# Kernel optimization log

Hardware: AMD Instinct MI355X
Metric: run time of the kernel (lower is better)

The kernel has to match this reference:

```python
import jax, jax.numpy as jnp
import numpy as np
from functools import partial

DIM, HID, DK, NH, SEQ, B = 1024, 512, 512, 4, 16, 2048
DH = DK // NH  # per-head dim = 128
EPS = 1e-5


def _ln(x, g, b):
    m = x.mean(-1, keepdims=True)
    v = ((x - m) ** 2).mean(-1, keepdims=True)
    return (x - m) * jax.lax.rsqrt(v + EPS) * g + b


def setup_inputs() -> dict:
    key = jax.random.key(0)
    ks = jax.random.split(key, 32)
    it = iter(range(32))
    n = lambda shape, s: jax.random.normal(ks[next(it)], shape, jnp.float32) * s
    inp = {
        'visual': n((B, SEQ, DIM), 1.0),
        'text':   n((B, SEQ, DIM), 1.0),
        'user':   n((B, SEQ, DIM), 1.0),
        'cat':    n((B, SEQ, DIM), 1.0),
        'label':  n((B, SEQ, 1), 1.0),
        'h0':     n((B, HID), 1.0),
        'c0':     n((B, HID), 1.0),
        # fusion MLP: Linear(4*dim -> dim)
        'fus_W': n((DIM, 4 * DIM), 1.0 / np.sqrt(4 * DIM)),
        'fus_b': n((DIM,), 0.01),
        # LayerNormLSTM cell params (gate order i,f,g,o)
        'W_ih': n((4 * HID, DIM), 1.0 / np.sqrt(DIM)),
        'W_hh': n((4 * HID, HID), 1.0 / np.sqrt(HID)),
        'g_ih': 1.0 + n((4 * HID,), 0.1), 'b_ih': n((4 * HID,), 0.01),
        'g_hh': 1.0 + n((4 * HID,), 0.1), 'b_hh': n((4 * HID,), 0.01),
        'g_c':  1.0 + n((HID,), 0.1),     'b_c':  n((HID,), 0.01),
        # attention projections
        'wq_W': n((DK, HID), 1.0 / np.sqrt(HID)), 'wq_b': n((DK,), 0.01),
        'wk_W': n((DK, HID), 1.0 / np.sqrt(HID)), 'wk_b': n((DK,), 0.01),
        'wv_W': n((NH, DK, HID), 1.0 / np.sqrt(HID)), 'wv_b': n((NH, DK), 0.01),
        'wout_W': n((DK, DK * NH), 1.0 / np.sqrt(DK * NH)), 'wout_b': n((DK,), 0.01),
        'out_W': n((1, DK), 1.0 / np.sqrt(DK)), 'out_b': n((1,), 0.01),
    }
    return inp


def reference(visual, text, user, cat, label, h0, c0, fus_W, fus_b,
              W_ih, W_hh, g_ih, b_ih, g_hh, b_hh, g_c, b_c,
              wq_W, wq_b, wk_W, wk_b, wv_W, wv_b, wout_W, wout_b, out_W, out_b):
    # fusion MLP (dropout is identity at inference)
    mods = jnp.concatenate([visual, text, user, cat], axis=-1)  # [B,S,4*DIM]
    v_t = jax.nn.relu(mods @ fus_W.T + fus_b)                    # [B,S,DIM]

    # LayerNorm-LSTM recurrence over time via scan
    def step(carry, x_t):
        h, c = carry
        gates = _ln(x_t @ W_ih.T, g_ih, b_ih) + _ln(h @ W_hh.T, g_hh, b_hh)
        i, f, g, o = jnp.split(gates, 4, axis=-1)
        c = jax.nn.sigmoid(f) * c + jax.nn.sigmoid(i) * jnp.tanh(g)
        h = jax.nn.sigmoid(o) * jnp.tanh(_ln(c, g_c, b_c))
        return (h, c), h

    (hn, _), hs = jax.lax.scan(step, (h0, c0), jnp.swapaxes(v_t, 0, 1))
    lstm_out = jnp.swapaxes(hs, 0, 1)  # [B,S,HID]

    # multi-head dot self-attention against final hidden state
    q = (hn @ wq_W.T + wq_b).reshape(-1, NH, DH)                    # [B,H,dh]
    k = (lstm_out @ wk_W.T + wk_b).reshape(-1, SEQ, NH, DH)         # [B,S,H,dh]
    scores = jnp.einsum('bshd,bhd->bhs', k, q) / np.sqrt(DH)        # [B,H,S]
    attn = jax.nn.softmax(scores, axis=-1)
    # per-head full-width values: V[b,h,s,k]
    V = jnp.einsum('hkd,bsd->bhsk', wv_W, lstm_out) + wv_b[None, :, None, :]
    ctx = jnp.einsum('bhsk,bhs->bhk', V, attn).reshape(-1, NH * DK)  # [B,H*DK]
    out_h = ctx @ wout_W.T + wout_b                                  # [B,DK]
    output = out_h @ out_W.T + out_b                                 # [B,1]

    label_one = label[:, -1, 0]
    loss = jnp.mean((output.reshape(-1) - label_one) ** 2)
    return loss, output
```

## Files before the change

### kernel.cpp

```cpp
#include <hip/hip_runtime.h>
#include <cstdint>

#define B_SZ 2048
#define SEQ  16
#define DIM  1024
#define HID  512
#define DK   512
#define NH   4
#define DH   128
#define GATE 2048
#define EPSV 1e-5f

typedef __bf16 bf8_t __attribute__((ext_vector_type(8)));
typedef float  f4_t  __attribute__((ext_vector_type(4)));
typedef unsigned short u16x8 __attribute__((ext_vector_type(8)));
typedef unsigned short u16x4 __attribute__((ext_vector_type(4)));

__device__ __forceinline__ unsigned short f2bf(float f){
  __bf16 h = (__bf16)f;
  return __builtin_bit_cast(unsigned short, h);
}
__device__ __forceinline__ float bf2f(unsigned short u){
  return __builtin_bit_cast(float, ((unsigned int)u) << 16);
}
__device__ __forceinline__ float sigm(float x){ return 1.f/(1.f+__expf(-x)); }
__device__ __forceinline__ float tanh_f(float x){ return 1.f - 2.f/(__expf(2.f*x)+1.f); }

__device__ __forceinline__ void gload16(const void* g, void* l){
  __builtin_amdgcn_global_load_lds(
      (const __attribute__((address_space(1))) void*)g,
      (__attribute__((address_space(3))) void*)l, 16, 0, 0);
}

template<bool OUT_BF16, bool BIAS, bool RELU>
__global__ __launch_bounds__(512, 1) void gemm8p(
    const unsigned short* __restrict__ A,
    const unsigned short* __restrict__ Bw,
    const float* __restrict__ bias,
    void* __restrict__ Cp,
    int N, int K, int nwg)
{
  __shared__ __align__(16) unsigned short As[2][256*64];
  __shared__ __align__(16) unsigned short Bs[2][256*64];
  const int tid = threadIdx.x, lane = tid & 63, w = tid >> 6;
  const int bid = blockIdx.x;
  const int swz = (bid & 7)*(nwg >> 3) + (bid >> 3);
  const int nx  = N >> 8;
  const int lnx = 31 - __clz(nx);
  const int bm0 = (swz >> lnx) << 8;
  const int bn0 = (swz & (nx-1)) << 8;

  const int l8  = lane >> 3;
  const int gsw = (lane & 7) ^ l8;
  const int fr  = lane & 15, kg = lane >> 4;
  const int wm  = (w >> 2)*128, wn = (w & 3)*64;
  const int KT  = K >> 6;

  auto stA = [&](int buf, int kt, int h){
    #pragma unroll
    for (int c=0;c<2;++c){
      const int rb = h*128 + c*64 + w*8;
      gload16(A + (size_t)(bm0 + rb + l8)*K + (size_t)kt*64 + gsw*8, &As[buf][rb*64]);
    }
  };
  auto stB = [&](int buf, int kt, int h){
    #pragma unroll
    for (int c=0;c<2;++c){
      const int rb = h*128 + c*64 + w*8;
      gload16(Bw + (size_t)(bn0 + rb + l8)*K + (size_t)kt*64 + gsw*8, &Bs[buf][rb*64]);
    }
  };
  auto rdA = [&](int buf, int m, int kk)->bf8_t{
    return *(const bf8_t*)&As[buf][(wm + m*16 + fr)*64 + (((kk*4+kg) ^ (fr&7))*8)];
  };
  auto rdB = [&](int buf, int n, int kk)->bf8_t{
    return *(const bf8_t*)&Bs[buf][(wn + n*16 + fr)*64 + (((kk*4+kg) ^ (fr&7))*8)];
  };

  f4_t acc[8][4];
  #pragma unroll
  for (int m=0;m<8;++m)
    #pragma unroll
    for (int n=0;n<4;++n) acc[m][n] = (f4_t)0.f;

  bf8_t bfr[4][2];

  auto mfma2 = [&](int m0, const bf8_t a00, const bf8_t a01,
                   const bf8_t a10, const bf8_t a11){
    __builtin_amdgcn_s_setprio(1);
    #pragma unroll
    for (int n=0;n<4;++n){
      acc[m0][n]   = __builtin_amdgcn_mfma_f32_16x16x32_bf16(a00, bfr[n][0], acc[m0][n],   0,0,0);
      acc[m0][n]   = __builtin_amdgcn_mfma_f32_16x16x32_bf16(a01, bfr[n][1], acc[m0][n],   0,0,0);
      acc[m0+1][n] = __builtin_amdgcn_mfma_f32_16x16x32_bf16(a10, bfr[n][0], acc[m0+1][n], 0,0,0);
      acc[m0+1][n] = __builtin_amdgcn_mfma_f32_16x16x32_bf16(a11, bfr[n][1], acc[m0+1][n], 0,0,0);
    }
    __builtin_amdgcn_s_setprio(0);
  };

  auto phase12 = [&](int buf, auto&& stg){
    #pragma unroll
    for (int n=0;n<4;++n){ bfr[n][0]=rdB(buf,n,0); bfr[n][1]=rdB(buf,n,1); }
    const bf8_t a00=rdA(buf,0,0), a01=rdA(buf,0,1), a10=rdA(buf,1,0), a11=rdA(buf,1,1);
    stg();
    asm volatile("s_barrier" ::: "memory");
    mfma2(0, a00,a01,a10,a11);
    asm volatile("s_barrier" ::: "memory");
  };
  auto phase4 = [&](int buf, int m0, auto&& stg, bool vm){
    const bf8_t a00=rdA(buf,m0,0), a01=rdA(buf,m0,1), a10=rdA(buf,m0+1,0), a11=rdA(buf,m0+1,1);
    stg();
    if (vm){
      __builtin_amdgcn_sched_barrier(0);
      asm volatile("s_waitcnt vmcnt(4)" ::: "memory");
    }
    asm volatile("s_barrier" ::: "memory");
    mfma2(m0, a00,a01,a10,a11);
    asm volatile("s_barrier" ::: "memory");
  };

  stA(0,0,0); stA(0,0,1); stB(0,0,0); stB(0,0,1);
  stB(1,1,0); stB(1,1,1);
  __builtin_amdgcn_sched_barrier(0);
  asm volatile("s_waitcnt vmcnt(4)" ::: "memory");
  asm volatile("s_barrier" ::: "memory");

  const int NIT = KT >> 1;
  for (int it=0; it<NIT; ++it){
    const int t0 = 2*it, t1 = t0+1;
    const int tN  = (t0+2 < KT) ? t0+2 : KT-1;
    const int tB3 = (t1+2 < KT) ? t1+2 : KT-1;

    phase12(0,      [&]{ stA(1,t1,0);  });
    phase4 (0, 2,   [&]{ stA(1,t1,1);  }, false);
    phase4 (0, 4,   [&]{ stB(0,tN,0);  }, false);
    phase4 (0, 6,   [&]{ stB(0,tN,1);  }, true);
    phase12(1,      [&]{ stA(0,tN,0);  });
    phase4 (1, 2,   [&]{ stA(0,tN,1);  }, false);
    phase4 (1, 4,   [&]{ stB(1,tB3,0); }, false);
    phase4 (1, 6,   [&]{ stB(1,tB3,1); }, true);
  }

  #pragma unroll
  for (int n=0;n<4;++n){
    const int col = bn0 + wn + n*16 + fr;
    float bv = 0.f;
    if constexpr (BIAS) bv = bias[col];
    #pragma unroll
    for (int m=0;m<8;++m){
      #pragma unroll
      for (int j=0;j<4;++j){
        const int row = bm0 + wm + m*16 + kg*4 + j;
        float v = acc[m][n][j] + bv;
        if constexpr (RELU) v = fmaxf(v, 0.f);
        if constexpr (OUT_BF16) ((unsigned short*)Cp)[(size_t)row*N + col] = f2bf(v);
        else                    ((float*)Cp)[(size_t)row*N + col] = v;
      }
    }
  }
}

template<bool OUT_BF16, bool BIAS>
__global__ __launch_bounds__(256) void gemm64(
    const unsigned short* __restrict__ A,
    const unsigned short* __restrict__ Bw,
    const float* __restrict__ bias,
    void* __restrict__ Cp,
    int N, int K, int nwg)
{
  __shared__ __align__(16) unsigned short As[64*64];
  __shared__ __align__(16) unsigned short Bs[64*64];
  const int tid = threadIdx.x, lane = tid & 63, wave = tid >> 6;
  const int bid = blockIdx.x;
  const int swz = (bid & 7)*(nwg >> 3) + (bid >> 3);
  const int nx  = N >> 6;
  const int lnx = 31 - __clz(nx);
  const int bm0 = (swz >> lnx) << 6;
  const int bn0 = (swz & (nx-1)) << 6;

  const int r8  = lane >> 3;
  const int gsw = ((lane & 7) ^ r8) * 8;
  const unsigned short* Ab = A  + (size_t)(bm0 + wave*16 + r8)*K + gsw;
  const unsigned short* Bb = Bw + (size_t)(bn0 + wave*16 + r8)*K + gsw;
  unsigned short* la = As + wave*1024;
  unsigned short* lb = Bs + wave*1024;

  f4_t acc[2][2];
  #pragma unroll
  for (int m=0;m<2;++m)
    #pragma unroll
    for (int n=0;n<2;++n) acc[m][n] = (f4_t)0.f;

  const int KT = K >> 6;
  const int fr = lane & 15, kg = lane >> 4;
  const int wm = (wave & 1)*32, wn = (wave >> 1)*32;

  for (int kt = 0; kt < KT; ++kt){
    if (kt) __syncthreads();
    const size_t ko = (size_t)kt*64;
    #pragma unroll
    for (int q = 0; q < 2; ++q){
      gload16(Ab + ko + (size_t)q*8*K, la + q*512);
      gload16(Bb + ko + (size_t)q*8*K, lb + q*512);
    }
    __syncthreads();
    #pragma unroll
    for (int kk = 0; kk < 2; ++kk){
      bf8_t af[2], bf_[2];
      #pragma unroll
      for (int m=0;m<2;++m){
        const int r = wm+m*16+fr;
        af[m]  = *(const bf8_t*)&As[r*64 + (((kk*4+kg) ^ (r&7))*8)];
      }
      #pragma unroll
      for (int n=0;n<2;++n){
        const int r = wn+n*16+fr;
        bf_[n] = *(const bf8_t*)&Bs[r*64 + (((kk*4+kg) ^ (r&7))*8)];
      }
      #pragma unroll
      for (int m=0;m<2;++m)
        #pragma unroll
        for (int n=0;n<2;++n)
          acc[m][n] = __builtin_amdgcn_mfma_f32_16x16x32_bf16(af[m], bf_[n], acc[m][n], 0,0,0);
    }
  }

  #pragma unroll
  for (int n=0;n<2;++n){
    const int col = bn0 + wn + n*16 + fr;
    float bv = 0.f;
    if constexpr (BIAS) bv = bias[col];
    #pragma unroll
    for (int m=0;m<2;++m){
      #pragma unroll
      for (int j=0;j<4;++j){
        const int row = bm0 + wm + m*16 + kg*4 + j;
        float v = acc[m][n][j] + bv;
        if constexpr (OUT_BF16) ((unsigned short*)Cp)[(size_t)row*N + col] = f2bf(v);
        else                    ((float*)Cp)[(size_t)row*N + col] = v;
      }
    }
  }
}

__global__ __launch_bounds__(256) void lstm_step(
  const unsigned short* __restrict__ X, const unsigned short* __restrict__ Gh,
  const float* __restrict__ c_src, float* __restrict__ c_dst,
  const float* __restrict__ g_ih, const float* __restrict__ b_ih,
  const float* __restrict__ g_hh, const float* __restrict__ b_hh,
  const float* __restrict__ g_c,  const float* __restrict__ b_c,
  unsigned short* __restrict__ h_out, unsigned short* __restrict__ lstm_out,
  int t)
{
  const int b = blockIdx.x, tid = threadIdx.x;
  __shared__ float xs[GATE];
  __shared__ float gs[GATE];
  __shared__ float red[32];
  const unsigned short* xrow = X  + ((size_t)b*SEQ + t)*GATE;
  const unsigned short* grow = Gh + (size_t)b*GATE;
  u16x8 xv = *(const u16x8*)&xrow[tid*8];
  u16x8 gv = *(const u16x8*)&grow[tid*8];
  float sx=0,sx2=0,sg=0,sg2=0;
  #pragma unroll
  for (int j=0;j<8;++j){
    float x = bf2f(xv[j]), g = bf2f(gv[j]);
    xs[tid*8+j]=x; gs[tid*8+j]=g;
    sx += x; sx2 += x*x; sg += g; sg2 += g*g;
  }
  #pragma unroll
  for (int m=32;m;m>>=1){
    sx += __shfl_xor(sx,m); sx2 += __shfl_xor(sx2,m);
    sg += __shfl_xor(sg,m); sg2 += __shfl_xor(sg2,m);
  }
  const int w = tid>>6;
  if ((tid&63)==0){ red[w]=sx; red[4+w]=sx2; red[8+w]=sg; red[12+w]=sg2; }
  __syncthreads();
  sx  = red[0]+red[1]+red[2]+red[3];
  sx2 = red[4]+red[5]+red[6]+red[7];
  sg  = red[8]+red[9]+red[10]+red[11];
  sg2 = red[12]+red[13]+red[14]+red[15];
  const float mX = sx*(1.f/GATE), mH = sg*(1.f/GATE);
  const float rX = rsqrtf(sx2*(1.f/GATE)-mX*mX+EPSV);
  const float rH = rsqrtf(sg2*(1.f/GATE)-mH*mH+EPSV);

  float cN[2], xo[2]; float sc=0, sc2=0;
  #pragma unroll
  for (int rep=0;rep<2;++rep){
    const int n = tid + rep*256;
    const int ni=n, nf=n+HID, ng=n+2*HID, no=n+3*HID;
    float gi = (xs[ni]-mX)*rX*g_ih[ni]+b_ih[ni] + (gs[ni]-mH)*rH*g_hh[ni]+b_hh[ni];
    float gf = (xs[nf]-mX)*rX*g_ih[nf]+b_ih[nf] + (gs[nf]-mH)*rH*g_hh[nf]+b_hh[nf];
    float gg = (xs[ng]-mX)*rX*g_ih[ng]+b_ih[ng] + (gs[ng]-mH)*rH*g_hh[ng]+b_hh[ng];
    float go = (xs[no]-mX)*rX*g_ih[no]+b_ih[no] + (gs[no]-mH)*rH*g_hh[no]+b_hh[no];
    float co = c_src[(size_t)b*HID + n];
    float cn = sigm(gf)*co + sigm(gi)*tanh_f(gg);
    cN[rep]=cn; xo[rep]=go;
    sc += cn; sc2 += cn*cn;
  }
  #pragma unroll
  for (int m=32;m;m>>=1){ sc += __shfl_xor(sc,m); sc2 += __shfl_xor(sc2,m); }
  if ((tid&63)==0){ red[16+w]=sc; red[20+w]=sc2; }
  __syncthreads();
  sc  = red[16]+red[17]+red[18]+red[19];
  sc2 = red[20]+red[21]+red[22]+red[23];
  const float mC = sc*(1.f/HID);
  const float rC = rsqrtf(sc2*(1.f/HID)-mC*mC+EPSV);
  #pragma unroll
  for (int rep=0;rep<2;++rep){
    const int n = tid + rep*256;
    float hN = sigm(xo[rep])*tanh_f((cN[rep]-mC)*rC*g_c[n]+b_c[n]);
    c_dst[(size_t)b*HID+n] = cN[rep];
    unsigned short hbv = f2bf(hN);
    h_out[(size_t)b*HID+n] = hbv;
    lstm_out[((size_t)b*SEQ+t)*HID+n] = hbv;
  }
}

__global__ __launch_bounds__(256) void attn_out_k(
  const float* __restrict__ q, const unsigned short* __restrict__ Km,
  const unsigned short* __restrict__ lo_all,
  const float* __restrict__ u, const float* __restrict__ Cc,
  float* __restrict__ out)
{
  const int b = blockIdx.x, tid = threadIdx.x;
  __shared__ float qs[DK];
  __shared__ float sc[NH][SEQ];
  __shared__ float at[NH][SEQ];
  __shared__ float red[4];
  for (int i=tid; i<DK; i+=256) qs[i] = q[(size_t)b*DK + i];
  __syncthreads();
  {
    const int p = tid>>2, sub = tid&3, h = p>>4, s = p&15;
    const unsigned short* krow = Km + ((size_t)b*SEQ + s)*DK + h*DH + sub*32;
    const float* qh = &qs[h*DH + sub*32];
    float part = 0.f;
    #pragma unroll
    for (int c8=0;c8<4;++c8){
      u16x8 kv = *(const u16x8*)(krow + c8*8);
      #pragma unroll
      for (int j=0;j<8;++j) part += qh[c8*8+j]*bf2f(kv[j]);
    }
    part += __shfl_xor(part,1); part += __shfl_xor(part,2);
    if (sub==0) sc[h][s] = part * 0.08838834764831845f;
  }
  __syncthreads();
  if (tid < 64){
    const int h = tid>>4;
    float v = sc[h][tid&15], mx = v;
    #pragma unroll
    for (int m=1;m<16;m<<=1) mx = fmaxf(mx, __shfl_xor(mx,m));
    float e = __expf(v-mx), se = e;
    #pragma unroll
    for (int m=1;m<16;m<<=1) se += __shfl_xor(se,m);
    at[h][tid&15] = e/se;
  }
  __syncthreads();
  float accum = 0.f;
  #pragma unroll
  for (int it=0; it<4; ++it){
    const int idx = it*256 + tid;
    const int h = idx>>8, d0 = (idx&255)*2;
    const unsigned short* lo = lo_all + (size_t)b*SEQ*HID + d0;
    float p0=0.f, p1=0.f;
    #pragma unroll
    for (int s=0;s<16;++s){
      unsigned int pr = *(const unsigned int*)(lo + s*HID);
      float a = at[h][s];
      p0 += a*bf2f((unsigned short)(pr&0xffffu));
      p1 += a*bf2f((unsigned short)(pr>>16));
    }
    accum += u[h*HID+d0]*p0 + u[h*HID+d0+1]*p1;
  }
  #pragma unroll
  for (int m=32;m;m>>=1) accum += __shfl_xor(accum,m);
  if ((tid&63)==0) red[tid>>6] = accum;
  __syncthreads();
  if (tid==0) out[1+b] = red[0]+red[1]+red[2]+red[3] + Cc[0];
}

__global__ __launch_bounds__(256) void loss_k(const float* __restrict__ label, float* __restrict__ out){
  const int tid = threadIdx.x;
  __shared__ float red[4];
  float s = 0.f;
  for (int b=tid; b<B_SZ; b+=256){
    float d = out[1+b] - label[(size_t)b*SEQ + (SEQ-1)];
    s += d*d;
  }
  #pragma unroll
  for (int m=32;m;m>>=1) s += __shfl_xor(s,m);
  if ((tid&63)==0) red[tid>>6]=s;
  __syncthreads();
  if (tid==0) out[0] = (red[0]+red[1]+red[2]+red[3]) * (1.f/B_SZ);
}

__global__ __launch_bounds__(256) void cvt_bf16_k(const float* __restrict__ in, unsigned short* __restrict__ o, int n){
  int i = (blockIdx.x*256 + threadIdx.x)*4;
  if (i < n){
    f4_t v = *(const f4_t*)&in[i];
    u16x4 w;
    #pragma unroll
    for (int j=0;j<4;++j) w[j] = f2bf(v[j]);
    *(u16x4*)&o[i] = w;
  }
}

__global__ __launch_bounds__(256) void cvt4_k(
  const float* __restrict__ v0, const float* __restrict__ v1,
  const float* __restrict__ v2, const float* __restrict__ v3,
  unsigned short* __restrict__ dst)
{
  const int idx = blockIdx.x*256 + threadIdx.x;
  const int src = blockIdx.y;
  const float* s = src==0?v0 : src==1?v1 : src==2?v2 : v3;
  const size_t e0 = (size_t)idx*8;
  const int row = (int)(e0 >> 10);
  const int col = (int)(e0 & 1023);
  f4_t a = *(const f4_t*)&s[e0];
  f4_t b = *(const f4_t*)&s[e0+4];
  u16x8 w;
  #pragma unroll
  for (int j=0;j<4;++j){ w[j]=f2bf(a[j]); w[4+j]=f2bf(b[j]); }
  *(u16x8*)&dst[(size_t)row*4096 + src*1024 + col] = w;
}

__global__ __launch_bounds__(256) void fold_we_k(
  const float* __restrict__ wout_W, const float* __restrict__ out_W, float* __restrict__ we)
{
  const int j = blockIdx.x*256 + threadIdx.x;
  float s=0.f;
  for (int m=0;m<512;++m) s += out_W[m]*wout_W[(size_t)m*2048+j];
  we[j]=s;
}
__global__ __launch_bounds__(256) void fold_u_k(
  const float* __restrict__ we, const float* __restrict__ wv_W, float* __restrict__ u)
{
  const int o = blockIdx.x*256 + threadIdx.x;
  const int h = o>>9, d = o&511;
  const float* wv = wv_W + (size_t)h*262144 + d;
  const float* wp = we + h*512;
  float s=0.f;
  for (int k=0;k<512;++k) s += wp[k]*wv[(size_t)k*512];
  u[o]=s;
}
__global__ __launch_bounds__(256) void fold_c_k(
  const float* __restrict__ we, const float* __restrict__ wv_b,
  const float* __restrict__ out_W, const float* __restrict__ wout_b,
  const float* __restrict__ out_b, float* __restrict__ Cc)
{
  const int tid = threadIdx.x;
  __shared__ float red[4];
  float s=0.f;
  for (int j=tid;j<2048;j+=256) s += we[j]*wv_b[j];
  for (int m=tid;m<512;m+=256)  s += out_W[m]*wout_b[m];
  #pragma unroll
  for (int m=32;m;m>>=1) s += __shfl_xor(s,m);
  if ((tid&63)==0) red[tid>>6]=s;
  __syncthreads();
  if (tid==0) Cc[0] = red[0]+red[1]+red[2]+red[3] + out_b[0];
}

extern "C" void kernel_launch(void* const* d_in, const int* in_sizes, int n_in,
                              void* d_out, int out_size, void* d_ws, size_t ws_size,
                              hipStream_t stream)
{
  const float* visual = (const float*)d_in[0];
  const float* text   = (const float*)d_in[1];
  const float* user_  = (const float*)d_in[2];
  const float* cat_   = (const float*)d_in[3];
  const float* label  = (const float*)d_in[4];
  const float* h0     = (const float*)d_in[5];
  const float* c0     = (const float*)d_in[6];
  const float* fus_W  = (const float*)d_in[7];
  const float* fus_b  = (const float*)d_in[8];
  const float* W_ih   = (const float*)d_in[9];
  const float* W_hh   = (const float*)d_in[10];
  const float* g_ih   = (const float*)d_in[11];
  const float* b_ih   = (const float*)d_in[12];
  const float* g_hh   = (const float*)d_in[13];
  const float* b_hh   = (const float*)d_in[14];
  const float* g_c    = (const float*)d_in[15];
  const float* b_c    = (const float*)d_in[16];
  const float* wq_W   = (const float*)d_in[17];
  const float* wq_b   = (const float*)d_in[18];
  const float* wk_W   = (const float*)d_in[19];
  const float* wk_b   = (const float*)d_in[20];
  const float* wv_W   = (const float*)d_in[21];
  const float* wv_b   = (const float*)d_in[22];
  const float* wout_W = (const float*)d_in[23];
  const float* wout_b = (const float*)d_in[24];
  const float* out_W  = (const float*)d_in[25];
  const float* out_b  = (const float*)d_in[26];
  (void)in_sizes; (void)n_in; (void)out_size; (void)ws_size;

  char* base = (char*)d_ws; size_t off = 0;
  auto alloc = [&](size_t n)->void*{ void* p = base+off; off += n; off = (off+255)&~(size_t)255; return p; };
  unsigned short* modsB = (unsigned short*)alloc((size_t)32768*4096*2);
  unsigned short* X     = modsB;
  unsigned short* vt    = (unsigned short*)alloc((size_t)32768*1024*2);
  unsigned short* lo    = (unsigned short*)alloc((size_t)32768*512*2);
  unsigned short* Km    = (unsigned short*)alloc((size_t)32768*512*2);
  unsigned short* Gh    = (unsigned short*)alloc((size_t)2048*2048*2);
  float*          cws   = (float*)         alloc((size_t)2048*512*4);
  unsigned short* hb    = (unsigned short*)alloc((size_t)2048*512*2);
  float*          qb    = (float*)         alloc((size_t)2048*512*4);
  unsigned short* fusWb = (unsigned short*)alloc((size_t)1024*4096*2);
  unsigned short* Wihb  = (unsigned short*)alloc((size_t)2048*1024*2);
  unsigned short* Whhb  = (unsigned short*)alloc((size_t)2048*512*2);
  unsigned short* wqb   = (unsigned short*)alloc((size_t)512*512*2);
  unsigned short* wkb   = (unsigned short*)alloc((size_t)512*512*2);
  float*          we_ws = (float*)         alloc(2048*4);
  float*          u_ws  = (float*)         alloc(2048*4);
  float*          C_ws  = (float*)         alloc(256);

  cvt4_k<<<dim3(16384,4), dim3(256), 0, stream>>>(visual, text, user_, cat_, modsB);
  cvt_bf16_k<<<dim3(4096), dim3(256), 0, stream>>>(fus_W, fusWb, 1024*4096);
  cvt_bf16_k<<<dim3(2048), dim3(256), 0, stream>>>(W_ih,  Wihb,  2048*1024);
  cvt_bf16_k<<<dim3(1024), dim3(256), 0, stream>>>(W_hh,  Whhb,  2048*512);
  cvt_bf16_k<<<dim3(256),  dim3(256), 0, stream>>>(wq_W,  wqb,   512*512);
  cvt_bf16_k<<<dim3(256),  dim3(256), 0, stream>>>(wk_W,  wkb,   512*512);
  cvt_bf16_k<<<dim3(1024), dim3(256), 0, stream>>>(h0,    hb,    2048*512);
  fold_we_k<<<dim3(8), dim3(256), 0, stream>>>(wout_W, out_W, we_ws);
  fold_u_k <<<dim3(8), dim3(256), 0, stream>>>(we_ws, wv_W, u_ws);
  fold_c_k <<<dim3(1), dim3(256), 0, stream>>>(we_ws, wv_b, out_W, wout_b, out_b, C_ws);

  gemm8p<true,true,true><<<dim3(512), dim3(512), 0, stream>>>(
      modsB, fusWb, fus_b, vt, 1024, 4096, 512);
  gemm8p<true,false,false><<<dim3(1024), dim3(512), 0, stream>>>(
      vt, Wihb, nullptr, X, 2048, 1024, 1024);

  for (int t=0; t<SEQ; ++t){
    gemm64<true,false><<<dim3(1024), dim3(256), 0, stream>>>(
        hb, Whhb, nullptr, Gh, 2048, 512, 1024);
    lstm_step<<<dim3(2048), dim3(256), 0, stream>>>(
        X, Gh, (t==0 ? c0 : cws), cws, g_ih, b_ih, g_hh, b_hh, g_c, b_c, hb, lo, t);
  }

  gemm64<false,true><<<dim3(256), dim3(256), 0, stream>>>(
      hb, wqb, wq_b, qb, 512, 512, 256);
  gemm8p<true,true,false><<<dim3(256), dim3(512), 0, stream>>>(
      lo, wkb, wk_b, Km, 512, 512, 256);

  attn_out_k<<<dim3(2048), dim3(256), 0, stream>>>(qb, Km, lo, u_ws, C_ws, (float*)d_out);
  loss_k<<<dim3(1), dim3(256), 0, stream>>>(label, (float*)d_out);
}
```

Measured before the change: 1.004 ms.

## Fuse fp32-to-bf16 modality concat conversion into fusion GEMM A-tile loads

Drops the separate kernel that converted the four fp32 modality inputs into a concatenated bf16 buffer. The fusion GEMM now reads fp32 A tiles straight from the four source tensors through registers, converts them to bf16 and writes them into swizzled LDS inside the pipelined main loop. This removes one large write and re-read of a 32768x4096 bf16 intermediate. In exchange the GEMM reads A as fp32, which doubles A global traffic per tile, and adds register pressure plus conversion work to the pipeline.

Result: faster. 978.3 us (-2.6%).

```diff
diff --git a/kernel.cpp b/kernel.cpp
--- a/kernel.cpp
+++ b/kernel.cpp
@@ -155,6 +155,148 @@
         if constexpr (RELU) v = fmaxf(v, 0.f);
         if constexpr (OUT_BF16) ((unsigned short*)Cp)[(size_t)row*N + col] = f2bf(v);
         else                    ((float*)Cp)[(size_t)row*N + col] = v;
+      }
+    }
+  }
+}
+
+__global__ __launch_bounds__(512, 1) void gemm8pf(
+    const float* __restrict__ A0, const float* __restrict__ A1,
+    const float* __restrict__ A2, const float* __restrict__ A3,
+    const unsigned short* __restrict__ Bw,
+    const float* __restrict__ bias,
+    unsigned short* __restrict__ Cp,
+    int N, int K, int nwg)
+{
+  __shared__ __align__(16) unsigned short As[2][256*64];
+  __shared__ __align__(16) unsigned short Bs[2][256*64];
+  const int tid = threadIdx.x, lane = tid & 63, w = tid >> 6;
+  const int bid = blockIdx.x;
+  const int swz = (bid & 7)*(nwg >> 3) + (bid >> 3);
+  const int nx  = N >> 8;
+  const int lnx = 31 - __clz(nx);
+  const int bm0 = (swz >> lnx) << 8;
+  const int bn0 = (swz & (nx-1)) << 8;
+
+  const int l8  = lane >> 3;
+  const int gsw = (lane & 7) ^ l8;
+  const int fr  = lane & 15, kg = lane >> 4;
+  const int wm  = (w >> 2)*128, wn = (w & 3)*64;
+  const int KT  = K >> 6;
+
+  auto stB = [&](int buf, int kt, int h){
+    #pragma unroll
+    for (int c=0;c<2;++c){
+      const int rb = h*128 + c*64 + w*8;
+      gload16(Bw + (size_t)(bn0 + rb + l8)*K + (size_t)kt*64 + gsw*8, &Bs[buf][rb*64]);
+    }
+  };
+
+  f4_t rg[4];
+  auto ldA = [&](int kt, int h){
+    const int kb = kt*64, si = kb >> 10, kc = kb & 1023;
+    const float* Asel = si==0?A0 : si==1?A1 : si==2?A2 : A3;
+    const float* p = Asel + (size_t)(bm0 + h*128 + (tid>>2))*1024 + kc + (tid&3)*16;
+    rg[0] = *(const f4_t*)p;     rg[1] = *(const f4_t*)(p+4);
+    rg[2] = *(const f4_t*)(p+8); rg[3] = *(const f4_t*)(p+12);
+  };
+  auto wrA = [&](int buf, int h){
+    const int row = h*128 + (tid>>2);
+    const int s = row & 7, g0 = (tid&3)*2;
+    u16x8 w0, w1;
+    #pragma unroll
+    for (int j=0;j<4;++j){
+      w0[j]=f2bf(rg[0][j]); w0[4+j]=f2bf(rg[1][j]);
+      w1[j]=f2bf(rg[2][j]); w1[4+j]=f2bf(rg[3][j]);
+    }
+    *(u16x8*)&As[buf][row*64 + ((g0^s)*8)]     = w0;
+    *(u16x8*)&As[buf][row*64 + (((g0+1)^s)*8)] = w1;
+  };
+
+  auto rdA = [&](int buf, int m, int kk)->bf8_t{
+    return *(const bf8_t*)&As[buf][(wm + m*16 + fr)*64 + (((kk*4+kg) ^ (fr&7))*8)];
+  };
+  auto rdB = [&](int buf, int n, int kk)->bf8_t{
+    return *(const bf8_t*)&Bs[buf][(wn + n*16 + fr)*64 + (((kk*4+kg) ^ (fr&7))*8)];
+  };
+
+  f4_t acc[8][4];
+  #pragma unroll
+  for (int m=0;m<8;++m)
+    #pragma unroll
+    for (int n=0;n<4;++n) acc[m][n] = (f4_t)0.f;
+
+  bf8_t bfr[4][2];
+
+  auto mfma2 = [&](int m0, const bf8_t a00, const bf8_t a01,
+                   const bf8_t a10, const bf8_t a11){
+    __builtin_amdgcn_s_setprio(1);
+    #pragma unroll
+    for (int n=0;n<4;++n){
+      acc[m0][n]   = __builtin_amdgcn_mfma_f32_16x16x32_bf16(a00, bfr[n][0], acc[m0][n],   0,0,0);
+      acc[m0][n]   = __builtin_amdgcn_mfma_f32_16x16x32_bf16(a01, bfr[n][1], acc[m0][n],   0,0,0);
+      acc[m0+1][n] = __builtin_amdgcn_mfma_f32_16x16x32_bf16(a10, bfr[n][0], acc[m0+1][n], 0,0,0);
+      acc[m0+1][n] = __builtin_amdgcn_mfma_f32_16x16x32_bf16(a11, bfr[n][1], acc[m0+1][n], 0,0,0);
+    }
+    __builtin_amdgcn_s_setprio(0);
+  };
+
+  auto phase12 = [&](int buf, auto&& stg){
+    #pragma unroll
+    for (int n=0;n<4;++n){ bfr[n][0]=rdB(buf,n,0); bfr[n][1]=rdB(buf,n,1); }
+    const bf8_t a00=rdA(buf,0,0), a01=rdA(buf,0,1), a10=rdA(buf,1,0), a11=rdA(buf,1,1);
+    stg();
+    asm volatile("s_barrier" ::: "memory");
+    mfma2(0, a00,a01,a10,a11);
+    asm volatile("s_barrier" ::: "memory");
+  };
+  auto phase4 = [&](int buf, int m0, auto&& stg, bool vm){
+    const bf8_t a00=rdA(buf,m0,0), a01=rdA(buf,m0,1), a10=rdA(buf,m0+1,0), a11=rdA(buf,m0+1,1);
+    stg();
+    if (vm){
+      __builtin_amdgcn_sched_barrier(0);
+      asm volatile("s_waitcnt vmcnt(4)" ::: "memory");
+    }
+    asm volatile("s_barrier" ::: "memory");
+    mfma2(m0, a00,a01,a10,a11);
+    asm volatile("s_barrier" ::: "memory");
+  };
+
+  stB(0,0,0); stB(0,0,1); stB(1,1,0); stB(1,1,1);
+  ldA(0,0); wrA(0,0); ldA(0,1); wrA(0,1);
+  asm volatile("s_waitcnt lgkmcnt(0)" ::: "memory");
+  asm volatile("s_waitcnt vmcnt(0)" ::: "memory");
+  asm volatile("s_barrier" ::: "memory");
+
+  const int NIT = KT >> 1;
+  for (int it=0; it<NIT; ++it){
+    const int t0 = 2*it, t1 = t0+1;
+    const int tN  = (t0+2 < KT) ? t0+2 : KT-1;
+    const int tB3 = (t1+2 < KT) ? t1+2 : KT-1;
+
+    phase12(0,      [&]{ ldA(t1,0); });
+    phase4 (0, 2,   [&]{ wrA(1,0); ldA(t1,1); }, false);
+    phase4 (0, 4,   [&]{ wrA(1,1); stB(0,tN,0); }, false);
+    phase4 (0, 6,   [&]{ stB(0,tN,1);
+                         asm volatile("s_waitcnt lgkmcnt(0)":::"memory"); }, true);
+    phase12(1,      [&]{ ldA(tN,0); });
+    phase4 (1, 2,   [&]{ wrA(0,0); ldA(tN,1); }, false);
+    phase4 (1, 4,   [&]{ wrA(0,1); stB(1,tB3,0); }, false);
+    phase4 (1, 6,   [&]{ stB(1,tB3,1);
+                         asm volatile("s_waitcnt lgkmcnt(0)":::"memory"); }, true);
+  }
+
+  #pragma unroll
+  for (int n=0;n<4;++n){
+    const int col = bn0 + wn + n*16 + fr;
+    const float bv = bias[col];
+    #pragma unroll
+    for (int m=0;m<8;++m){
+      #pragma unroll
+      for (int j=0;j<4;++j){
+        const int row = bm0 + wm + m*16 + kg*4 + j;
+        float v = fmaxf(acc[m][n][j] + bv, 0.f);
+        Cp[(size_t)row*N + col] = f2bf(v);
       }
     }
   }
@@ -402,25 +544,6 @@
     for (int j=0;j<4;++j) w[j] = f2bf(v[j]);
     *(u16x4*)&o[i] = w;
   }
-}
-
-__global__ __launch_bounds__(256) void cvt4_k(
-  const float* __restrict__ v0, const float* __restrict__ v1,
-  const float* __restrict__ v2, const float* __restrict__ v3,
-  unsigned short* __restrict__ dst)
-{
-  const int idx = blockIdx.x*256 + threadIdx.x;
-  const int src = blockIdx.y;
-  const float* s = src==0?v0 : src==1?v1 : src==2?v2 : v3;
-  const size_t e0 = (size_t)idx*8;
-  const int row = (int)(e0 >> 10);
-  const int col = (int)(e0 & 1023);
-  f4_t a = *(const f4_t*)&s[e0];
-  f4_t b = *(const f4_t*)&s[e0+4];
-  u16x8 w;
-  #pragma unroll
-  for (int j=0;j<4;++j){ w[j]=f2bf(a[j]); w[4+j]=f2bf(b[j]); }
-  *(u16x8*)&dst[(size_t)row*4096 + src*1024 + col] = w;
 }
 
 __global__ __launch_bounds__(256) void fold_we_k(
@@ -494,8 +617,7 @@
 
   char* base = (char*)d_ws; size_t off = 0;
   auto alloc = [&](size_t n)->void*{ void* p = base+off; off += n; off = (off+255)&~(size_t)255; return p; };
-  unsigned short* modsB = (unsigned short*)alloc((size_t)32768*4096*2);
-  unsigned short* X     = modsB;
+  unsigned short* X     = (unsigned short*)alloc((size_t)32768*2048*2);
   unsigned short* vt    = (unsigned short*)alloc((size_t)32768*1024*2);
   unsigned short* lo    = (unsigned short*)alloc((size_t)32768*512*2);
   unsigned short* Km    = (unsigned short*)alloc((size_t)32768*512*2);
@@ -512,7 +634,6 @@
   float*          u_ws  = (float*)         alloc(2048*4);
   float*          C_ws  = (float*)         alloc(256);
 
-  cvt4_k<<<dim3(16384,4), dim3(256), 0, stream>>>(visual, text, user_, cat_, modsB);
   cvt_bf16_k<<<dim3(4096), dim3(256), 0, stream>>>(fus_W, fusWb, 1024*4096);
   cvt_bf16_k<<<dim3(2048), dim3(256), 0, stream>>>(W_ih,  Wihb,  2048*1024);
   cvt_bf16_k<<<dim3(1024), dim3(256), 0, stream>>>(W_hh,  Whhb,  2048*512);
@@ -523,8 +644,8 @@
   fold_u_k <<<dim3(8), dim3(256), 0, stream>>>(we_ws, wv_W, u_ws);
   fold_c_k <<<dim3(1), dim3(256), 0, stream>>>(we_ws, wv_b, out_W, wout_b, out_b, C_ws);
 
-  gemm8p<true,true,true><<<dim3(512), dim3(512), 0, stream>>>(
-      modsB, fusWb, fus_b, vt, 1024, 4096, 512);
+  gemm8pf<<<dim3(512), dim3(512), 0, stream>>>(
+      visual, text, user_, cat_, fusWb, fus_b, vt, 1024, 4096, 512);
   gemm8p<true,false,false><<<dim3(1024), dim3(512), 0, stream>>>(
       vt, Wihb, nullptr, X, 2048, 1024, 1024);
 
```
